# Kernel optimization log

Measured on AMD Instinct MI355X. Metric: run time of the kernel, lower is better.

The kernel has to match this reference:

```python
import jax, jax.numpy as jnp
import numpy as np

MARGIN = 1.0


def setup_inputs() -> dict:
    key = jax.random.key(0)
    k1, k2 = jax.random.split(key)
    embeddings = jax.random.normal(k1, (512, 128), dtype=jnp.float32)
    labels = jax.random.randint(k2, (512,), 0, 64)
    return {"embeddings": embeddings, "labels": labels}


def reference(embeddings, labels):
    # embeddings: [B, D], labels: [B]
    B = embeddings.shape[0]

    # Pairwise squared distances, same math as the gathered (a-p)^2 sums:
    # D[i, j] = ||e_i - e_j||^2, shape [B, B]
    diff = embeddings[:, None, :] - embeddings[None, :, :]  # [B, B, D]
    dist = jnp.sum(diff * diff, axis=-1)                    # [B, B]

    # Valid-pair masks (distinct indices; same / different labels).
    diff_index = ~jnp.eye(B, dtype=bool)
    same_label = labels[:, None] == labels[None, :]
    pos_mask = diff_index & same_label    # valid (a, p)
    neg_mask = diff_index & ~same_label   # valid (a, n)

    # Valid triplet mask [a, p, n].
    triplet_mask = pos_mask[:, :, None] & neg_mask[:, None, :]

    # relu(d(a,p) - d(a,n) + margin) over all triplets, mean over valid ones
    # (equivalent to enumerating nonzero mask entries and gathering).
    terms = jax.nn.relu(dist[:, :, None] - dist[:, None, :] + MARGIN)  # [B,B,B]
    loss_sum = jnp.sum(jnp.where(triplet_mask, terms, 0.0))
    count = jnp.sum(triplet_mask).astype(embeddings.dtype)
    return loss_sum / count
```

## Files before the change

kernel.cpp:

```cpp
#include <hip/hip_runtime.h>

#define BATCH 512
#define DIM 128
#define MARGIN 1.0f

__global__ __launch_bounds__(256) void triplet_main_kernel(
    const float* __restrict__ emb, const int* __restrict__ labels,
    double* __restrict__ loss_part, int* __restrict__ cnt_part)
{
    const int a = blockIdx.x;
    const int tid = threadIdx.x;

    __shared__ float ea[DIM];
    __shared__ float drow[BATCH];
    __shared__ float posd[BATCH];
    __shared__ int lbls[BATCH];
    __shared__ int npos;
    __shared__ float rsum[256];
    __shared__ int rcnt[256];

    if (tid < DIM) ea[tid] = emb[a * DIM + tid];
    if (tid == 0) npos = 0;
    for (int j = tid; j < BATCH; j += 256) lbls[j] = labels[j];
    __syncthreads();

    const int la = lbls[a];

    const float4* eav = reinterpret_cast<const float4*>(ea);
    for (int j = tid; j < BATCH; j += 256) {
        const float4* ej = reinterpret_cast<const float4*>(emb + (size_t)j * DIM);
        float acc = 0.f;
        #pragma unroll
        for (int d4 = 0; d4 < DIM / 4; ++d4) {
            float4 vj = ej[d4];
            float4 va = eav[d4];
            float dx = va.x - vj.x;
            float dy = va.y - vj.y;
            float dz = va.z - vj.z;
            float dw = va.w - vj.w;
            acc += dx * dx + dy * dy + dz * dz + dw * dw;
        }
        drow[j] = acc;
    }
    __syncthreads();

    for (int j = tid; j < BATCH; j += 256) {
        if (j != a && lbls[j] == la) {
            int idx = atomicAdd(&npos, 1);
            posd[idx] = drow[j];
        }
    }
    __syncthreads();

    const int np = npos;

    float lsum = 0.f;
    int lcnt = 0;
    for (int n = tid; n < BATCH; n += 256) {
        if (lbls[n] != la) {
            const float dan_m = MARGIN - drow[n];
            for (int p = 0; p < np; ++p) {
                float t = posd[p] + dan_m;
                lsum += (t > 0.f) ? t : 0.f;
            }
            lcnt += np;
        }
    }

    rsum[tid] = lsum;
    rcnt[tid] = lcnt;
    __syncthreads();
    for (int s = 128; s > 0; s >>= 1) {
        if (tid < s) {
            rsum[tid] += rsum[tid + s];
            rcnt[tid] += rcnt[tid + s];
        }
        __syncthreads();
    }
    if (tid == 0) {
        loss_part[a] = (double)rsum[0];
        cnt_part[a] = rcnt[0];
    }
}

__global__ __launch_bounds__(512) void triplet_finalize_kernel(
    const double* __restrict__ loss_part, const int* __restrict__ cnt_part,
    float* __restrict__ out)
{
    __shared__ double s[BATCH];
    __shared__ long long c[BATCH];
    const int t = threadIdx.x;
    s[t] = loss_part[t];
    c[t] = (long long)cnt_part[t];
    __syncthreads();
    for (int st = 256; st > 0; st >>= 1) {
        if (t < st) {
            s[t] += s[t + st];
            c[t] += c[t + st];
        }
        __syncthreads();
    }
    if (t == 0) out[0] = (float)(s[0] / (double)c[0]);
}

extern "C" void kernel_launch(void* const* d_in, const int* in_sizes, int n_in,
                              void* d_out, int out_size, void* d_ws, size_t ws_size,
                              hipStream_t stream) {
    const float* emb = (const float*)d_in[0];
    const int* labels = (const int*)d_in[1];
    float* out = (float*)d_out;

    double* loss_part = (double*)d_ws;
    int* cnt_part = (int*)((char*)d_ws + BATCH * sizeof(double));

    triplet_main_kernel<<<BATCH, 256, 0, stream>>>(emb, labels, loss_part, cnt_part);
    triplet_finalize_kernel<<<1, BATCH, 0, stream>>>(loss_part, cnt_part, out);
}
```

Baseline: 25.27 us.

## Fuse finalize into main kernel via fixed-point atomics and last-block ticket

Removes the separate finalize kernel: each block adds its partial loss as a fixed-point 64-bit integer and its triplet count via global atomics, and the last block (by ticket counter) computes the final mean. Positive-distance compaction is now done with wave ballots instead of shared-memory atomics, and the block reduction uses wave shuffles. This saves a kernel launch and a reduction pass but adds a hipMemsetAsync on the workspace and fixed-point rounding of the loss sum.

```diff
diff --git a/kernel.cpp b/kernel.cpp
--- a/kernel.cpp
+++ b/kernel.cpp
@@ -3,24 +3,29 @@
 #define BATCH 512
 #define DIM 128
 #define MARGIN 1.0f
+#define FXSCALE 1048576.0
 
-__global__ __launch_bounds__(256) void triplet_main_kernel(
+
+__global__ __launch_bounds__(256) void triplet_fused_kernel(
     const float* __restrict__ emb, const int* __restrict__ labels,
-    double* __restrict__ loss_part, int* __restrict__ cnt_part)
+    unsigned long long* __restrict__ acc_loss,
+    unsigned long long* __restrict__ acc_count,
+    unsigned int* __restrict__ ticket,
+    float* __restrict__ out)
 {
     const int a = blockIdx.x;
     const int tid = threadIdx.x;
+    const int lane = tid & 63;
+    const int wv = tid >> 6;
 
     __shared__ float ea[DIM];
     __shared__ float drow[BATCH];
     __shared__ float posd[BATCH];
     __shared__ int lbls[BATCH];
-    __shared__ int npos;
-    __shared__ float rsum[256];
-    __shared__ int rcnt[256];
+    __shared__ int s_np, s_nneg;
+    __shared__ float wsum[4];
 
     if (tid < DIM) ea[tid] = emb[a * DIM + tid];
-    if (tid == 0) npos = 0;
     for (int j = tid; j < BATCH; j += 256) lbls[j] = labels[j];
     __syncthreads();
 
@@ -44,18 +49,28 @@
     }
     __syncthreads();
 
-    for (int j = tid; j < BATCH; j += 256) {
-        if (j != a && lbls[j] == la) {
-            int idx = atomicAdd(&npos, 1);
-            posd[idx] = drow[j];
+    if (wv == 0) {
+        int np = 0, nsame = 0;
+        for (int base = 0; base < BATCH; base += 64) {
+            int j = base + lane;
+            bool same = (lbls[j] == la);
+            bool pos = same && (j != a);
+            unsigned long long pmask = __ballot(pos);
+            if (pos) {
+                int idx = np + __popcll(pmask & ((1ull << lane) - 1ull));
+                posd[idx] = drow[j];
+            }
+            np += __popcll(pmask);
+            nsame += __popcll(__ballot(same));
         }
+        if (lane == 0) { s_np = np; s_nneg = BATCH - nsame; }
     }
     __syncthreads();
 
-    const int np = npos;
+    const int np = s_np;
+    const int nneg = s_nneg;
 
     float lsum = 0.f;
-    int lcnt = 0;
     for (int n = tid; n < BATCH; n += 256) {
         if (lbls[n] != la) {
             const float dan_m = MARGIN - drow[n];
@@ -63,44 +78,28 @@
                 float t = posd[p] + dan_m;
                 lsum += (t > 0.f) ? t : 0.f;
             }
-            lcnt += np;
         }
     }
 
-    rsum[tid] = lsum;
-    rcnt[tid] = lcnt;
+    #pragma unroll
+    for (int off = 32; off > 0; off >>= 1) lsum += __shfl_down(lsum, off, 64);
+    if (lane == 0) wsum[wv] = lsum;
     __syncthreads();
-    for (int s = 128; s > 0; s >>= 1) {
-        if (tid < s) {
-            rsum[tid] += rsum[tid + s];
-            rcnt[tid] += rcnt[tid + s];
+
+    if (tid == 0) {
+        double tot = (double)wsum[0] + (double)wsum[1] + (double)wsum[2] + (double)wsum[3];
+        long long fx = llround(tot * FXSCALE);
+        atomicAdd(acc_loss, (unsigned long long)fx);
+        atomicAdd(acc_count, (unsigned long long)((long long)np * nneg));
+        __threadfence();
+        unsigned int prev = atomicAdd(ticket, 1u);
+        if (prev == BATCH - 1) {
+            __threadfence();
+            unsigned long long L = atomicAdd(acc_loss, 0ull);
+            unsigned long long C = atomicAdd(acc_count, 0ull);
+            out[0] = (float)(((double)L / FXSCALE) / (double)C);
         }
-        __syncthreads();
     }
-    if (tid == 0) {
-        loss_part[a] = (double)rsum[0];
-        cnt_part[a] = rcnt[0];
-    }
-}
-
-__global__ __launch_bounds__(512) void triplet_finalize_kernel(
-    const double* __restrict__ loss_part, const int* __restrict__ cnt_part,
-    float* __restrict__ out)
-{
-    __shared__ double s[BATCH];
-    __shared__ long long c[BATCH];
-    const int t = threadIdx.x;
-    s[t] = loss_part[t];
-    c[t] = (long long)cnt_part[t];
-    __syncthreads();
-    for (int st = 256; st > 0; st >>= 1) {
-        if (t < st) {
-            s[t] += s[t + st];
-            c[t] += c[t + st];
-        }
-        __syncthreads();
-    }
-    if (t == 0) out[0] = (float)(s[0] / (double)c[0]);
 }
 
 extern "C" void kernel_launch(void* const* d_in, const int* in_sizes, int n_in,
@@ -110,9 +109,12 @@
     const int* labels = (const int*)d_in[1];
     float* out = (float*)d_out;
 
-    double* loss_part = (double*)d_ws;
-    int* cnt_part = (int*)((char*)d_ws + BATCH * sizeof(double));
+    unsigned long long* acc_loss = (unsigned long long*)d_ws;
+    unsigned long long* acc_count = (unsigned long long*)((char*)d_ws + 8);
+    unsigned int* ticket = (unsigned int*)((char*)d_ws + 16);
 
-    triplet_main_kernel<<<BATCH, 256, 0, stream>>>(emb, labels, loss_part, cnt_part);
-    triplet_finalize_kernel<<<1, BATCH, 0, stream>>>(loss_part, cnt_part, out);
+    hipMemsetAsync(d_ws, 0, 24, stream);
+
+    triplet_fused_kernel<<<BATCH, 256, 0, stream>>>(emb, labels, acc_loss, acc_count,
+                                                    ticket, out);
 }
```

After: 47.21 us. 1.87x slower.
